# Kernel tuning notes

Measured on AMD Instinct MI355X. Metric: run time of the kernel, lower is better.

Reference implementation:

```python
import jax, jax.numpy as jnp
import numpy as np

N = 20000
E = 320000
IN_FEAT = 256
HID = 256
OUT_FEAT = 128


def setup_inputs() -> dict:
    key = jax.random.key(0)
    ks = jax.random.split(key, 10)
    inp = {
        "x": jax.random.normal(ks[0], (N, IN_FEAT), dtype=jnp.float32),
        "edge_src": jax.random.randint(ks[1], (E,), 0, N, dtype=jnp.int32),
        "edge_dst": jax.random.randint(ks[2], (E,), 0, N, dtype=jnp.int32),
        "edge_w": jax.random.uniform(ks[3], (E,), dtype=jnp.float32),
        # params (Linear weights stored as [out, in], torch convention)
        "W_emb": jax.random.normal(ks[4], (HID, IN_FEAT), dtype=jnp.float32) / np.sqrt(IN_FEAT),
        "W_gc1": jax.random.normal(ks[5], (HID, 2 * HID), dtype=jnp.float32) / np.sqrt(2 * HID),
        "b_gc1": jnp.zeros((HID,), dtype=jnp.float32),
        "W_gc2": jax.random.normal(ks[6], (HID, 2 * HID), dtype=jnp.float32) / np.sqrt(2 * HID),
        "b_gc2": jnp.zeros((HID,), dtype=jnp.float32),
        "W_fc": jax.random.normal(ks[7], (OUT_FEAT, HID), dtype=jnp.float32) / np.sqrt(HID),
    }
    return inp


def reference(x, edge_src, edge_dst, edge_w, W_emb, W_gc1, b_gc1, W_gc2, b_gc2, W_fc):
    n = x.shape[0]

    def adj_mul(h):
        msgs = h[edge_src] * edge_w[:, None]           # [E, hid]
        return jax.ops.segment_sum(msgs, edge_dst, num_segments=n)

    def gconv(h, W, b):
        cat = jnp.concatenate([h, adj_mul(h)], axis=1)  # [N, 2*hid]
        return cat @ W.T + b

    h = x @ W_emb.T                                    # embedding (no bias)
    h = h + jax.nn.relu(gconv(h, W_gc1, b_gc1))        # residual (dropout = eval identity)
    h = h + jax.nn.relu(gconv(h, W_gc2, b_gc2))
    out = h @ W_fc.T                                   # fc_last (no bias)
    out = out / jnp.sqrt(jnp.sum(out * out, axis=1, keepdims=True))
    return out
```

## Files before the change

### kernel.cpp

```cpp
#include <hip/hip_runtime.h>
#include <math.h>

#define N_NODES 20000
#define E_EDGES 320000
#define HID 256
#define OUT_FEAT 128
#define MPAD 20224
#define CAP 64

#define BK 64
#define LSTR 72
#define ISTR 80
#define TSTR 264

typedef __attribute__((ext_vector_type(8))) __bf16 bf16x8;
typedef __attribute__((ext_vector_type(4))) float floatx4;
typedef __attribute__((ext_vector_type(4))) int intx4;

__device__ __forceinline__ void write_int8_shadow(
    const __bf16 (*tile)[TSTR], int row0, int tid,
    unsigned char* __restrict__ h8, float* __restrict__ scl) {
    const int row = tid >> 3;
    const int seg = tid & 7;
    float vals[32];
    float mx = 0.f;
#pragma unroll
    for (int j = 0; j < 32; j++) {
        float v = (float)tile[row][seg * 32 + j];
        vals[j] = v;
        mx = fmaxf(mx, fabsf(v));
    }
#pragma unroll
    for (int m = 1; m <= 4; m <<= 1) mx = fmaxf(mx, __shfl_xor(mx, m));
    const float enc = mx > 0.f ? 127.f / mx : 0.f;
    unsigned int pk[8];
#pragma unroll
    for (int g = 0; g < 8; g++) {
        unsigned int wd = 0;
#pragma unroll
        for (int j = 0; j < 4; j++) {
            int q = (int)rintf(vals[g * 4 + j] * enc);
            q = q > 127 ? 127 : (q < -127 ? -127 : q);
            wd |= ((unsigned int)(q & 0xff)) << (8 * j);
        }
        pk[g] = wd;
    }
    unsigned char* dstp = h8 + (size_t)(row0 + row) * HID + seg * 32;
    *(int4*)dstp        = make_int4(pk[0], pk[1], pk[2], pk[3]);
    *(int4*)(dstp + 16) = make_int4(pk[4], pk[5], pk[6], pk[7]);
    if (seg == 0) scl[row0 + row] = mx * (1.f / 127.f);
}


#define EMB_BLK 316
#define SCAT_BLK 625
#define CONVL_BLK 40
#define CONVR_BLK 64

__global__ __launch_bounds__(512) void front_kernel(
    const float* __restrict__ x, const float* __restrict__ wembf,
    __bf16* __restrict__ hb0, unsigned char* __restrict__ h8, float* __restrict__ scl,
    const int* __restrict__ src, const int* __restrict__ dst,
    const float* __restrict__ w, int* __restrict__ counts, int2* __restrict__ edges,
    const float* __restrict__ w1f, const float* __restrict__ w2f, const float* __restrict__ wfcf,
    __bf16* __restrict__ w1l, __bf16* __restrict__ w2l, __bf16* __restrict__ wfcb,
    unsigned char* __restrict__ w1r8, unsigned char* __restrict__ w2r8,
    float* __restrict__ w1rs, float* __restrict__ w2rs)
{
    __shared__ char smem[64 * 144 + 256 * 144];
    const int bid = blockIdx.x;
    const int tid = threadIdx.x;

    if (bid < EMB_BLK) {
        __bf16* As = (__bf16*)smem;
        __bf16* Bs = (__bf16*)(smem + 64 * 144);
        const int row0 = bid * 64;
        const int wv = tid >> 6, l = tid & 63, lr = l & 15, lq = l >> 4;
        const int wm = wv & 1, wn4 = wv >> 1;

        floatx4 acc[2][4];
#pragma unroll
        for (int i = 0; i < 2; i++)
#pragma unroll
            for (int j = 0; j < 4; j++) acc[i][j] = (floatx4){0.f, 0.f, 0.f, 0.f};

        const int srow = tid >> 3;
        const int skq = (tid & 7) * 8;

        for (int kc = 0; kc < 256; kc += BK) {
            {
                int grow = row0 + srow;
                float4 v0 = make_float4(0.f, 0.f, 0.f, 0.f), v1 = v0;
                if (grow < N_NODES) {
                    const float* xp = x + (size_t)grow * HID + kc + skq;
                    v0 = *(const float4*)xp;
                    v1 = *(const float4*)(xp + 4);
                }
                bf16x8 o;
                o[0] = (__bf16)v0.x; o[1] = (__bf16)v0.y; o[2] = (__bf16)v0.z; o[3] = (__bf16)v0.w;
                o[4] = (__bf16)v1.x; o[5] = (__bf16)v1.y; o[6] = (__bf16)v1.z; o[7] = (__bf16)v1.w;
                *(bf16x8*)&As[srow * LSTR + skq] = o;
            }
#pragma unroll
            for (int r = 0; r < 4; r++) {
                int row = r * 64 + srow;
                const float* wp = wembf + (size_t)row * 256 + kc + skq;
                float4 v0 = *(const float4*)wp;
                float4 v1 = *(const float4*)(wp + 4);
                bf16x8 o;
                o[0] = (__bf16)v0.x; o[1] = (__bf16)v0.y; o[2] = (__bf16)v0.z; o[3] = (__bf16)v0.w;
                o[4] = (__bf16)v1.x; o[5] = (__bf16)v1.y; o[6] = (__bf16)v1.z; o[7] = (__bf16)v1.w;
                *(bf16x8*)&Bs[row * LSTR + skq] = o;
            }
            __syncthreads();
#pragma unroll
            for (int s = 0; s < 2; s++) {
                bf16x8 af[2], bfr[4];
#pragma unroll
                for (int mt = 0; mt < 2; mt++)
                    af[mt] = *(const bf16x8*)&As[(wm * 32 + mt * 16 + lr) * LSTR + s * 32 + lq * 8];
#pragma unroll
                for (int nt = 0; nt < 4; nt++)
                    bfr[nt] = *(const bf16x8*)&Bs[(wn4 * 64 + nt * 16 + lr) * LSTR + s * 32 + lq * 8];
#pragma unroll
                for (int mt = 0; mt < 2; mt++)
#pragma unroll
                    for (int nt = 0; nt < 4; nt++)
                        acc[mt][nt] = __builtin_amdgcn_mfma_f32_16x16x32_bf16(af[mt], bfr[nt], acc[mt][nt], 0, 0, 0);
            }
            __syncthreads();
        }
        __bf16 (*tile)[TSTR] = (__bf16(*)[TSTR])smem;
#pragma unroll
        for (int nt = 0; nt < 4; nt++) {
            const int col = wn4 * 64 + nt * 16 + lr;
#pragma unroll
            for (int mt = 0; mt < 2; mt++) {
                const int lrow = wm * 32 + mt * 16 + lq * 4;
#pragma unroll
                for (int r = 0; r < 4; r++) {
                    float v = acc[mt][nt][r];
                    hb0[(size_t)(row0 + lrow + r) * HID + col] = (__bf16)v;
                    tile[lrow + r][col] = (__bf16)v;
                }
            }
        }
        __syncthreads();
        write_int8_shadow(tile, row0, tid, h8, scl);
    } else if (bid < EMB_BLK + SCAT_BLK) {
        int e = (bid - EMB_BLK) * 512 + tid;
        int d = dst[e];
        int p = atomicAdd(&counts[d], 1);
        edges[(size_t)d * CAP + p] = make_int2(src[e], __float_as_int(w[e]));
    } else if (bid < EMB_BLK + SCAT_BLK + CONVL_BLK) {
        const size_t gi = ((size_t)(bid - EMB_BLK - SCAT_BLK) * 512 + tid) * 8;
        const float* sp; __bf16* dp;
        if (gi < 65536) {
            size_t row = gi >> 8, k = gi & 255;
            sp = w1f + row * 512 + k; dp = w1l + gi;
        } else if (gi < 131072) {
            size_t off = gi - 65536, row = off >> 8, k = off & 255;
            sp = w2f + row * 512 + k; dp = w2l + off;
        } else {
            size_t off = gi - 131072;
            sp = wfcf + off; dp = wfcb + off;
        }
        float4 v0 = *(const float4*)sp;
        float4 v1 = *(const float4*)(sp + 4);
        bf16x8 o;
        o[0] = (__bf16)v0.x; o[1] = (__bf16)v0.y; o[2] = (__bf16)v0.z; o[3] = (__bf16)v0.w;
        o[4] = (__bf16)v1.x; o[5] = (__bf16)v1.y; o[6] = (__bf16)v1.z; o[7] = (__bf16)v1.w;
        *(bf16x8*)dp = o;
    } else {
        const int gw = (bid - EMB_BLK - SCAT_BLK - CONVL_BLK) * 8 + (tid >> 6);
        const int lane = tid & 63;
        const float* Wsrc = (gw < 256) ? w1f : w2f;
        unsigned char* d8 = (gw < 256) ? w1r8 : w2r8;
        float* ds = (gw < 256) ? w1rs : w2rs;
        const int r = gw & 255;
        float4 v = *(const float4*)(Wsrc + (size_t)r * 512 + 256 + lane * 4);
        float mx = fmaxf(fmaxf(fabsf(v.x), fabsf(v.y)), fmaxf(fabsf(v.z), fabsf(v.w)));
#pragma unroll
        for (int m = 1; m <= 32; m <<= 1) mx = fmaxf(mx, __shfl_xor(mx, m));
        const float enc = mx > 0.f ? 127.f / mx : 0.f;
        unsigned int wd = 0;
        float vv[4] = {v.x, v.y, v.z, v.w};
#pragma unroll
        for (int j = 0; j < 4; j++) {
            int q = (int)rintf(vv[j] * enc);
            q = q > 127 ? 127 : (q < -127 ? -127 : q);
            wd |= ((unsigned int)(q & 0xff)) << (8 * j);
        }
        *(unsigned int*)(d8 + (size_t)r * 256 + lane * 4) = wd;
        if (lane == 0) ds[r] = mx * (1.f / 127.f);
    }
}


__global__ __launch_bounds__(256) void aggregate_kernel(
    const unsigned char* __restrict__ h8, const float* __restrict__ scl,
    const int* __restrict__ counts,
    const int2* __restrict__ edges,
    unsigned char* __restrict__ agg8, float* __restrict__ ascl) {
    const int w = threadIdx.x >> 6, lane = threadIdx.x & 63;
    const int half = lane >> 5, lh = lane & 31;
    const int d = blockIdx.x * 8 + w * 2 + half;
    const size_t base = (size_t)d * CAP;
    const int cnt = counts[d];
    const int iters = (cnt + 15) >> 4;
    float acc[8];
#pragma unroll
    for (int q = 0; q < 8; q++) acc[q] = 0.f;

    for (int it = 0; it < iters; ++it) {
        const int jb = it * 16;
        const int2* ep = edges + base + jb;
        int4 eh[8];
#pragma unroll
        for (int u = 0; u < 8; u++) eh[u] = *(const int4*)(ep + u * 2);
        int sidx[16]; float ew[16];
#pragma unroll
        for (int u = 0; u < 8; u++) {
            const bool m0 = (jb + u * 2)     < cnt;
            const bool m1 = (jb + u * 2 + 1) < cnt;
            sidx[u * 2]     = m0 ? eh[u].x : 0;
            ew[u * 2]       = m0 ? __int_as_float(eh[u].y) : 0.f;
            sidx[u * 2 + 1] = m1 ? eh[u].z : 0;
            ew[u * 2 + 1]   = m1 ? __int_as_float(eh[u].w) : 0.f;
        }
        float ws[16];
#pragma unroll
        for (int u = 0; u < 16; u++) ws[u] = ew[u] * scl[sidx[u]];
        uint2 hv[16];
#pragma unroll
        for (int u = 0; u < 16; u++)
            hv[u] = *(const uint2*)(h8 + (size_t)sidx[u] * HID + lh * 8);
#pragma unroll
        for (int u = 0; u < 16; u++) {
            const unsigned int a = hv[u].x, b = hv[u].y;
            const float wu = ws[u];
            acc[0] = fmaf(wu, (float)(int)(signed char)(a),       acc[0]);
            acc[1] = fmaf(wu, (float)(int)(signed char)(a >> 8),  acc[1]);
            acc[2] = fmaf(wu, (float)(int)(signed char)(a >> 16), acc[2]);
            acc[3] = fmaf(wu, (float)(int)(signed char)(a >> 24), acc[3]);
            acc[4] = fmaf(wu, (float)(int)(signed char)(b),       acc[4]);
            acc[5] = fmaf(wu, (float)(int)(signed char)(b >> 8),  acc[5]);
            acc[6] = fmaf(wu, (float)(int)(signed char)(b >> 16), acc[6]);
            acc[7] = fmaf(wu, (float)(int)(signed char)(b >> 24), acc[7]);
        }
    }
    float mx = 0.f;
#pragma unroll
    for (int q = 0; q < 8; q++) mx = fmaxf(mx, fabsf(acc[q]));
#pragma unroll
    for (int m = 1; m <= 16; m <<= 1) mx = fmaxf(mx, __shfl_xor(mx, m));
    const float enc = mx > 0.f ? 127.f / mx : 0.f;
    unsigned int w0 = 0, w1v = 0;
#pragma unroll
    for (int j = 0; j < 4; j++) {
        int q0 = (int)rintf(acc[j] * enc);
        q0 = q0 > 127 ? 127 : (q0 < -127 ? -127 : q0);
        w0 |= ((unsigned int)(q0 & 0xff)) << (8 * j);
        int q1 = (int)rintf(acc[4 + j] * enc);
        q1 = q1 > 127 ? 127 : (q1 < -127 ? -127 : q1);
        w1v |= ((unsigned int)(q1 & 0xff)) << (8 * j);
    }
    *(uint2*)(agg8 + (size_t)d * HID + lh * 8) = make_uint2(w0, w1v);
    if (lh == 0) ascl[d] = mx * (1.f / 127.f);
}


template <bool LAST>
__global__ __launch_bounds__(512) void gconv_kernel(
    const __bf16* __restrict__ hp,
    const unsigned char* __restrict__ ag8, const float* __restrict__ ascl,
    const __bf16* __restrict__ Wl,
    const unsigned char* __restrict__ Wr8, const float* __restrict__ Wrs,
    const float* __restrict__ bias,
    __bf16* __restrict__ hn, unsigned char* __restrict__ h8, float* __restrict__ scl,
    const __bf16* __restrict__ Wfc, float* __restrict__ outp)
{
    __shared__ char smem[64 * 144 + 256 * 144];
    __bf16* As = (__bf16*)smem;
    __bf16* Bs = (__bf16*)(smem + 64 * 144);
    char* As8 = smem;
    char* Bs8 = smem + 64 * ISTR;
    const int tid = threadIdx.x;
    const int row0 = blockIdx.x * 64;
    const int wv = tid >> 6, l = tid & 63, lr = l & 15, lq = l >> 4;
    const int wm = wv & 1, wn4 = wv >> 1;

    floatx4 acc[2][4];
    intx4 acc8[2][4];
#pragma unroll
    for (int i = 0; i < 2; i++)
#pragma unroll
        for (int j = 0; j < 4; j++) {
            acc[i][j] = (floatx4){0.f, 0.f, 0.f, 0.f};
            acc8[i][j] = (intx4){0, 0, 0, 0};
        }

    const int srow = tid >> 3;
    const int skq = (tid & 7) * 8;

    for (int kc = 0; kc < 256; kc += BK) {
        *(bf16x8*)&As[srow * LSTR + skq] =
            *(const bf16x8*)(hp + (size_t)(row0 + srow) * HID + kc + skq);
#pragma unroll
        for (int r = 0; r < 4; r++) {
            int row = r * 64 + srow;
            *(bf16x8*)&Bs[row * LSTR + skq] =
                *(const bf16x8*)(Wl + (size_t)row * 256 + kc + skq);
        }
        __syncthreads();
#pragma unroll
        for (int s = 0; s < 2; s++) {
            bf16x8 af[2], bfr[4];
#pragma unroll
            for (int mt = 0; mt < 2; mt++)
                af[mt] = *(const bf16x8*)&As[(wm * 32 + mt * 16 + lr) * LSTR + s * 32 + lq * 8];
#pragma unroll
            for (int nt = 0; nt < 4; nt++)
                bfr[nt] = *(const bf16x8*)&Bs[(wn4 * 64 + nt * 16 + lr) * LSTR + s * 32 + lq * 8];
#pragma unroll
            for (int mt = 0; mt < 2; mt++)
#pragma unroll
                for (int nt = 0; nt < 4; nt++)
                    acc[mt][nt] = __builtin_amdgcn_mfma_f32_16x16x32_bf16(af[mt], bfr[nt], acc[mt][nt], 0, 0, 0);
        }
        __syncthreads();
    }

    for (int kc = 0; kc < 256; kc += BK) {
        {
            int row = tid >> 3, sg = (tid & 7) * 8;
            *(uint2*)&As8[row * ISTR + sg] =
                *(const uint2*)(ag8 + (size_t)(row0 + row) * HID + kc + sg);
        }
#pragma unroll
        for (int rr = 0; rr < 2; rr++) {
            int idx = rr * 512 + tid;
            int row = idx >> 2, sg = (idx & 3) * 16;
            *(int4*)&Bs8[row * ISTR + sg] =
                *(const int4*)(Wr8 + (size_t)row * 256 + kc + sg);
        }
        __syncthreads();
        intx4 a8[2], b8[4];
#pragma unroll
        for (int mt = 0; mt < 2; mt++)
            a8[mt] = *(const intx4*)&As8[(wm * 32 + mt * 16 + lr) * ISTR + lq * 16];
#pragma unroll
        for (int nt = 0; nt < 4; nt++)
            b8[nt] = *(const intx4*)&Bs8[(wn4 * 64 + nt * 16 + lr) * ISTR + lq * 16];
#pragma unroll
        for (int mt = 0; mt < 2; mt++)
#pragma unroll
            for (int nt = 0; nt < 4; nt++)
                acc8[mt][nt] = __builtin_amdgcn_mfma_i32_16x16x64_i8(a8[mt], b8[nt], acc8[mt][nt], 0, 0, 0);
        __syncthreads();
    }

    __bf16 (*tile)[TSTR] = (__bf16(*)[TSTR])smem;
#pragma unroll
    for (int nt = 0; nt < 4; nt++) {
        const int col = wn4 * 64 + nt * 16 + lr;
        const float b = bias[col];
        const float wrc = Wrs[col];
#pragma unroll
        for (int mt = 0; mt < 2; mt++) {
            const int lrow = wm * 32 + mt * 16 + lq * 4;
#pragma unroll
            for (int r = 0; r < 4; r++) {
                const int row = row0 + lrow + r;
                float gem = acc[mt][nt][r] + (float)acc8[mt][nt][r] * (ascl[row] * wrc);
                float res = (float)hp[(size_t)row * HID + col];
                float v = res + fmaxf(gem + b, 0.f);
                if (!LAST) hn[(size_t)row * HID + col] = (__bf16)v;
                tile[lrow + r][col] = (__bf16)v;
            }
        }
    }
    __syncthreads();

    if (!LAST) {
        write_int8_shadow(tile, row0, tid, h8, scl);
    } else if (wv < 4) {
        floatx4 facc[8];
#pragma unroll
        for (int j = 0; j < 8; j++) facc[j] = (floatx4){0.f, 0.f, 0.f, 0.f};
#pragma unroll
        for (int kt = 0; kt < 256; kt += 32) {
            bf16x8 a = *(const bf16x8*)&tile[wv * 16 + lr][kt + lq * 8];
            bf16x8 bf8[8];
#pragma unroll
            for (int nt = 0; nt < 8; nt++)
                bf8[nt] = *(const bf16x8*)(Wfc + (size_t)(nt * 16 + lr) * 256 + kt + lq * 8);
#pragma unroll
            for (int nt = 0; nt < 8; nt++)
                facc[nt] = __builtin_amdgcn_mfma_f32_16x16x32_bf16(a, bf8[nt], facc[nt], 0, 0, 0);
        }
        float s[4];
#pragma unroll
        for (int r = 0; r < 4; r++) {
            float t = 0.f;
#pragma unroll
            for (int nt = 0; nt < 8; nt++) t = fmaf(facc[nt][r], facc[nt][r], t);
            s[r] = t;
        }
#pragma unroll
        for (int mask = 1; mask <= 8; mask <<= 1) {
#pragma unroll
            for (int r = 0; r < 4; r++) s[r] += __shfl_xor(s[r], mask);
        }
        float inv[4];
#pragma unroll
        for (int r = 0; r < 4; r++) inv[r] = rsqrtf(s[r]);
#pragma unroll
        for (int r = 0; r < 4; r++) {
            int row = row0 + wv * 16 + lq * 4 + r;
            if (row >= N_NODES) continue;
#pragma unroll
            for (int nt = 0; nt < 8; nt++)
                outp[(size_t)row * OUT_FEAT + nt * 16 + lr] = facc[nt][r] * inv[r];
        }
    }
}


extern "C" void kernel_launch(void* const* d_in, const int* in_sizes, int n_in,
                              void* d_out, int out_size, void* d_ws, size_t ws_size,
                              hipStream_t stream) {
    const float* x        = (const float*)d_in[0];
    const int*   edge_src = (const int*)d_in[1];
    const int*   edge_dst = (const int*)d_in[2];
    const float* edge_w   = (const float*)d_in[3];
    const float* W_emb    = (const float*)d_in[4];
    const float* W_gc1    = (const float*)d_in[5];
    const float* b_gc1    = (const float*)d_in[6];
    const float* W_gc2    = (const float*)d_in[7];
    const float* b_gc2    = (const float*)d_in[8];
    const float* W_fc     = (const float*)d_in[9];
    float* out = (float*)d_out;

    char* p = (char*)d_ws;
    const size_t HROW = (size_t)MPAD * HID;
    __bf16* hb0   = (__bf16*)p;             p += HROW * 2;
    __bf16* hb1   = (__bf16*)p;             p += HROW * 2;
    unsigned char* h8 = (unsigned char*)p;  p += HROW;
    float*  scl   = (float*)p;              p += (size_t)MPAD * 4;
    unsigned char* agg8 = (unsigned char*)p; p += HROW;
    float*  ascl  = (float*)p;              p += (size_t)MPAD * 4;
    __bf16* w1l   = (__bf16*)p;             p += 65536 * 2;
    __bf16* w2l   = (__bf16*)p;             p += 65536 * 2;
    __bf16* wfcb  = (__bf16*)p;             p += 32768 * 2;
    unsigned char* w1r8 = (unsigned char*)p; p += 65536;
    unsigned char* w2r8 = (unsigned char*)p; p += 65536;
    float*  w1rs  = (float*)p;              p += 256 * 4;
    float*  w2rs  = (float*)p;              p += 256 * 4;
    int2*   edges = (int2*)p;               p += (size_t)N_NODES * CAP * 8;
    int*    counts = (int*)p;               p += (size_t)MPAD * 4;

    hipMemsetAsync(counts, 0, (size_t)MPAD * 4, stream);

    front_kernel<<<EMB_BLK + SCAT_BLK + CONVL_BLK + CONVR_BLK, 512, 0, stream>>>(
        x, W_emb, hb0, h8, scl, edge_src, edge_dst, edge_w, counts, edges,
        W_gc1, W_gc2, W_fc, w1l, w2l, wfcb, w1r8, w2r8, w1rs, w2rs);

    aggregate_kernel<<<N_NODES / 8, 256, 0, stream>>>(h8, scl, counts, edges, agg8, ascl);

    gconv_kernel<false><<<MPAD / 64, 512, 0, stream>>>(
        hb0, agg8, ascl, w1l, w1r8, w1rs, b_gc1, hb1, h8, scl, nullptr, nullptr);

    aggregate_kernel<<<N_NODES / 8, 256, 0, stream>>>(h8, scl, counts, edges, agg8, ascl);

    gconv_kernel<true><<<MPAD / 64, 512, 0, stream>>>(
        hb1, agg8, ascl, w2l, w2r8, w2rs, b_gc2, nullptr, nullptr, nullptr, wfcb, out);
}
```

Baseline: 203.1 us.

## Fuse edge aggregation into gconv kernel and drop LDS staging for GEMM

Removes the separate aggregate kernels. Each gconv block now gathers and aggregates its own 32 destination rows, quantizes the result to int8 and writes it straight into shared memory as the A operand of the int8 MFMA, so the agg8/ascl global round trip and two launches go away. The dense GEMM operands (hp, Wl, Wr8) are now loaded directly from global memory into registers instead of being staged through LDS. The block shrinks to 32 rows and 256 threads with an occupancy hint, and ping-pong int8 shadow buffers avoid a read/write race across blocks. The cost is less weight reuse per block and more global/L2 traffic for the weights, and the irregular gather now runs in the same kernel as the MFMA work.

Result: slower. 207.6 us (+2.2%).

```diff
diff --git a/kernel.cpp b/kernel.cpp
--- a/kernel.cpp
+++ b/kernel.cpp
@@ -197,98 +197,101 @@
 }
 
 
-__global__ __launch_bounds__(256) void aggregate_kernel(
-    const unsigned char* __restrict__ h8, const float* __restrict__ scl,
-    const int* __restrict__ counts,
-    const int2* __restrict__ edges,
-    unsigned char* __restrict__ agg8, float* __restrict__ ascl) {
-    const int w = threadIdx.x >> 6, lane = threadIdx.x & 63;
-    const int half = lane >> 5, lh = lane & 31;
-    const int d = blockIdx.x * 8 + w * 2 + half;
-    const size_t base = (size_t)d * CAP;
-    const int cnt = counts[d];
-    const int iters = (cnt + 15) >> 4;
-    float acc[8];
-#pragma unroll
-    for (int q = 0; q < 8; q++) acc[q] = 0.f;
-
-    for (int it = 0; it < iters; ++it) {
-        const int jb = it * 16;
-        const int2* ep = edges + base + jb;
-        int4 eh[8];
-#pragma unroll
-        for (int u = 0; u < 8; u++) eh[u] = *(const int4*)(ep + u * 2);
-        int sidx[16]; float ew[16];
-#pragma unroll
-        for (int u = 0; u < 8; u++) {
-            const bool m0 = (jb + u * 2)     < cnt;
-            const bool m1 = (jb + u * 2 + 1) < cnt;
-            sidx[u * 2]     = m0 ? eh[u].x : 0;
-            ew[u * 2]       = m0 ? __int_as_float(eh[u].y) : 0.f;
-            sidx[u * 2 + 1] = m1 ? eh[u].z : 0;
-            ew[u * 2 + 1]   = m1 ? __int_as_float(eh[u].w) : 0.f;
-        }
-        float ws[16];
-#pragma unroll
-        for (int u = 0; u < 16; u++) ws[u] = ew[u] * scl[sidx[u]];
-        uint2 hv[16];
-#pragma unroll
-        for (int u = 0; u < 16; u++)
-            hv[u] = *(const uint2*)(h8 + (size_t)sidx[u] * HID + lh * 8);
-#pragma unroll
-        for (int u = 0; u < 16; u++) {
-            const unsigned int a = hv[u].x, b = hv[u].y;
-            const float wu = ws[u];
-            acc[0] = fmaf(wu, (float)(int)(signed char)(a),       acc[0]);
-            acc[1] = fmaf(wu, (float)(int)(signed char)(a >> 8),  acc[1]);
-            acc[2] = fmaf(wu, (float)(int)(signed char)(a >> 16), acc[2]);
-            acc[3] = fmaf(wu, (float)(int)(signed char)(a >> 24), acc[3]);
-            acc[4] = fmaf(wu, (float)(int)(signed char)(b),       acc[4]);
-            acc[5] = fmaf(wu, (float)(int)(signed char)(b >> 8),  acc[5]);
-            acc[6] = fmaf(wu, (float)(int)(signed char)(b >> 16), acc[6]);
-            acc[7] = fmaf(wu, (float)(int)(signed char)(b >> 24), acc[7]);
-        }
-    }
-    float mx = 0.f;
-#pragma unroll
-    for (int q = 0; q < 8; q++) mx = fmaxf(mx, fabsf(acc[q]));
-#pragma unroll
-    for (int m = 1; m <= 16; m <<= 1) mx = fmaxf(mx, __shfl_xor(mx, m));
-    const float enc = mx > 0.f ? 127.f / mx : 0.f;
-    unsigned int w0 = 0, w1v = 0;
-#pragma unroll
-    for (int j = 0; j < 4; j++) {
-        int q0 = (int)rintf(acc[j] * enc);
-        q0 = q0 > 127 ? 127 : (q0 < -127 ? -127 : q0);
-        w0 |= ((unsigned int)(q0 & 0xff)) << (8 * j);
-        int q1 = (int)rintf(acc[4 + j] * enc);
-        q1 = q1 > 127 ? 127 : (q1 < -127 ? -127 : q1);
-        w1v |= ((unsigned int)(q1 & 0xff)) << (8 * j);
-    }
-    *(uint2*)(agg8 + (size_t)d * HID + lh * 8) = make_uint2(w0, w1v);
-    if (lh == 0) ascl[d] = mx * (1.f / 127.f);
-}
-
+#define GBM 32
+#define AGG_BYTES (4 * GBM * ISTR)
+#define ASCL_OFF  AGG_BYTES
+#define GEMM_OFF  (AGG_BYTES + 128)
+#define TILE_BYTES (GBM * TSTR * 2)
 
 template <bool LAST>
-__global__ __launch_bounds__(512) void gconv_kernel(
+__global__ __launch_bounds__(256, 3) void gconv_kernel(
     const __bf16* __restrict__ hp,
-    const unsigned char* __restrict__ ag8, const float* __restrict__ ascl,
+    const unsigned char* __restrict__ h8in, const float* __restrict__ sclin,
+    const int* __restrict__ counts, const int2* __restrict__ edges,
     const __bf16* __restrict__ Wl,
     const unsigned char* __restrict__ Wr8, const float* __restrict__ Wrs,
     const float* __restrict__ bias,
-    __bf16* __restrict__ hn, unsigned char* __restrict__ h8, float* __restrict__ scl,
+    __bf16* __restrict__ hn, unsigned char* __restrict__ h8out, float* __restrict__ sclout,
     const __bf16* __restrict__ Wfc, float* __restrict__ outp)
 {
-    __shared__ char smem[64 * 144 + 256 * 144];
-    __bf16* As = (__bf16*)smem;
-    __bf16* Bs = (__bf16*)(smem + 64 * 144);
+    __shared__ char smem[GEMM_OFF + TILE_BYTES];
     char* As8 = smem;
-    char* Bs8 = smem + 64 * ISTR;
+    float* asclL = (float*)(smem + ASCL_OFF);
     const int tid = threadIdx.x;
-    const int row0 = blockIdx.x * 64;
+    const int row0 = blockIdx.x * GBM;
     const int wv = tid >> 6, l = tid & 63, lr = l & 15, lq = l >> 4;
-    const int wm = wv & 1, wn4 = wv >> 1;
+
+    {
+        const int hw = tid >> 5;
+        const int lh = tid & 31;
+#pragma unroll 1
+        for (int t = 0; t < 4; ++t) {
+            const int j = hw * 4 + t;
+            const int d = row0 + j;
+            const size_t base = (size_t)d * CAP;
+            const int cnt = counts[d];
+            const int iters = (cnt + 15) >> 4;
+            float acc[8];
+#pragma unroll
+            for (int q = 0; q < 8; q++) acc[q] = 0.f;
+
+            for (int it = 0; it < iters; ++it) {
+                const int jb = it * 16;
+                const int2* ep = edges + base + jb;
+                int4 eh[8];
+#pragma unroll
+                for (int u = 0; u < 8; u++) eh[u] = *(const int4*)(ep + u * 2);
+                int sidx[16]; float ew[16];
+#pragma unroll
+                for (int u = 0; u < 8; u++) {
+                    const bool m0 = (jb + u * 2)     < cnt;
+                    const bool m1 = (jb + u * 2 + 1) < cnt;
+                    sidx[u * 2]     = m0 ? eh[u].x : 0;
+                    ew[u * 2]       = m0 ? __int_as_float(eh[u].y) : 0.f;
+                    sidx[u * 2 + 1] = m1 ? eh[u].z : 0;
+                    ew[u * 2 + 1]   = m1 ? __int_as_float(eh[u].w) : 0.f;
+                }
+                float ws[16];
+#pragma unroll
+                for (int u = 0; u < 16; u++) ws[u] = ew[u] * sclin[sidx[u]];
+                uint2 hv[16];
+#pragma unroll
+                for (int u = 0; u < 16; u++)
+                    hv[u] = *(const uint2*)(h8in + (size_t)sidx[u] * HID + lh * 8);
+#pragma unroll
+                for (int u = 0; u < 16; u++) {
+                    const unsigned int a = hv[u].x, b = hv[u].y;
+                    const float wu = ws[u];
+                    acc[0] = fmaf(wu, (float)(int)(signed char)(a),       acc[0]);
+                    acc[1] = fmaf(wu, (float)(int)(signed char)(a >> 8),  acc[1]);
+                    acc[2] = fmaf(wu, (float)(int)(signed char)(a >> 16), acc[2]);
+                    acc[3] = fmaf(wu, (float)(int)(signed char)(a >> 24), acc[3]);
+                    acc[4] = fmaf(wu, (float)(int)(signed char)(b),       acc[4]);
+                    acc[5] = fmaf(wu, (float)(int)(signed char)(b >> 8),  acc[5]);
+                    acc[6] = fmaf(wu, (float)(int)(signed char)(b >> 16), acc[6]);
+                    acc[7] = fmaf(wu, (float)(int)(signed char)(b >> 24), acc[7]);
+                }
+            }
+            float mx = 0.f;
+#pragma unroll
+            for (int q = 0; q < 8; q++) mx = fmaxf(mx, fabsf(acc[q]));
+#pragma unroll
+            for (int m = 1; m <= 16; m <<= 1) mx = fmaxf(mx, __shfl_xor(mx, m));
+            const float enc = mx > 0.f ? 127.f / mx : 0.f;
+            unsigned int w0 = 0, w1v = 0;
+#pragma unroll
+            for (int jj = 0; jj < 4; jj++) {
+                int q0 = (int)rintf(acc[jj] * enc);
+                q0 = q0 > 127 ? 127 : (q0 < -127 ? -127 : q0);
+                w0 |= ((unsigned int)(q0 & 0xff)) << (8 * jj);
+                int q1 = (int)rintf(acc[4 + jj] * enc);
+                q1 = q1 > 127 ? 127 : (q1 < -127 ? -127 : q1);
+                w1v |= ((unsigned int)(q1 & 0xff)) << (8 * jj);
+            }
+            *(uint2*)&As8[(((lh >> 3) * GBM) + j) * ISTR + (lh & 7) * 8] = make_uint2(w0, w1v);
+            if (lh == 0) asclL[j] = mx * (1.f / 127.f);
+        }
+    }
 
     floatx4 acc[2][4];
     intx4 acc8[2][4];
@@ -300,79 +303,57 @@
             acc8[i][j] = (intx4){0, 0, 0, 0};
         }
 
-    const int srow = tid >> 3;
-    const int skq = (tid & 7) * 8;
-
+#pragma unroll
     for (int kc = 0; kc < 256; kc += BK) {
-        *(bf16x8*)&As[srow * LSTR + skq] =
-            *(const bf16x8*)(hp + (size_t)(row0 + srow) * HID + kc + skq);
-#pragma unroll
-        for (int r = 0; r < 4; r++) {
-            int row = r * 64 + srow;
-            *(bf16x8*)&Bs[row * LSTR + skq] =
-                *(const bf16x8*)(Wl + (size_t)row * 256 + kc + skq);
-        }
-        __syncthreads();
 #pragma unroll
         for (int s = 0; s < 2; s++) {
+            const int k0 = kc + s * 32 + lq * 8;
             bf16x8 af[2], bfr[4];
 #pragma unroll
             for (int mt = 0; mt < 2; mt++)
-                af[mt] = *(const bf16x8*)&As[(wm * 32 + mt * 16 + lr) * LSTR + s * 32 + lq * 8];
+                af[mt] = *(const bf16x8*)(hp + (size_t)(row0 + mt * 16 + lr) * HID + k0);
 #pragma unroll
             for (int nt = 0; nt < 4; nt++)
-                bfr[nt] = *(const bf16x8*)&Bs[(wn4 * 64 + nt * 16 + lr) * LSTR + s * 32 + lq * 8];
+                bfr[nt] = *(const bf16x8*)(Wl + (size_t)(wv * 64 + nt * 16 + lr) * 256 + k0);
 #pragma unroll
             for (int mt = 0; mt < 2; mt++)
 #pragma unroll
                 for (int nt = 0; nt < 4; nt++)
                     acc[mt][nt] = __builtin_amdgcn_mfma_f32_16x16x32_bf16(af[mt], bfr[nt], acc[mt][nt], 0, 0, 0);
         }
-        __syncthreads();
-    }
-
+    }
+
+    __syncthreads();
+
+#pragma unroll
     for (int kc = 0; kc < 256; kc += BK) {
-        {
-            int row = tid >> 3, sg = (tid & 7) * 8;
-            *(uint2*)&As8[row * ISTR + sg] =
-                *(const uint2*)(ag8 + (size_t)(row0 + row) * HID + kc + sg);
-        }
-#pragma unroll
-        for (int rr = 0; rr < 2; rr++) {
-            int idx = rr * 512 + tid;
-            int row = idx >> 2, sg = (idx & 3) * 16;
-            *(int4*)&Bs8[row * ISTR + sg] =
-                *(const int4*)(Wr8 + (size_t)row * 256 + kc + sg);
-        }
-        __syncthreads();
         intx4 a8[2], b8[4];
 #pragma unroll
         for (int mt = 0; mt < 2; mt++)
-            a8[mt] = *(const intx4*)&As8[(wm * 32 + mt * 16 + lr) * ISTR + lq * 16];
+            a8[mt] = *(const intx4*)&As8[(((kc >> 6) * GBM) + mt * 16 + lr) * ISTR + lq * 16];
 #pragma unroll
         for (int nt = 0; nt < 4; nt++)
-            b8[nt] = *(const intx4*)&Bs8[(wn4 * 64 + nt * 16 + lr) * ISTR + lq * 16];
+            b8[nt] = *(const intx4*)(Wr8 + (size_t)(wv * 64 + nt * 16 + lr) * 256 + kc + lq * 16);
 #pragma unroll
         for (int mt = 0; mt < 2; mt++)
 #pragma unroll
             for (int nt = 0; nt < 4; nt++)
                 acc8[mt][nt] = __builtin_amdgcn_mfma_i32_16x16x64_i8(a8[mt], b8[nt], acc8[mt][nt], 0, 0, 0);
-        __syncthreads();
-    }
-
-    __bf16 (*tile)[TSTR] = (__bf16(*)[TSTR])smem;
+    }
+
+    __bf16 (*tile)[TSTR] = (__bf16(*)[TSTR])(smem + GEMM_OFF);
 #pragma unroll
     for (int nt = 0; nt < 4; nt++) {
-        const int col = wn4 * 64 + nt * 16 + lr;
+        const int col = wv * 64 + nt * 16 + lr;
         const float b = bias[col];
         const float wrc = Wrs[col];
 #pragma unroll
         for (int mt = 0; mt < 2; mt++) {
-            const int lrow = wm * 32 + mt * 16 + lq * 4;
+            const int lrow = mt * 16 + lq * 4;
 #pragma unroll
             for (int r = 0; r < 4; r++) {
                 const int row = row0 + lrow + r;
-                float gem = acc[mt][nt][r] + (float)acc8[mt][nt][r] * (ascl[row] * wrc);
+                float gem = acc[mt][nt][r] + (float)acc8[mt][nt][r] * (asclL[lrow + r] * wrc);
                 float res = (float)hp[(size_t)row * HID + col];
                 float v = res + fmaxf(gem + b, 0.f);
                 if (!LAST) hn[(size_t)row * HID + col] = (__bf16)v;
@@ -383,8 +364,8 @@
     __syncthreads();
 
     if (!LAST) {
-        write_int8_shadow(tile, row0, tid, h8, scl);
-    } else if (wv < 4) {
+        write_int8_shadow(tile, row0, tid, h8out, sclout);
+    } else if (wv < 2) {
         floatx4 facc[8];
 #pragma unroll
         for (int j = 0; j < 8; j++) facc[j] = (floatx4){0.f, 0.f, 0.f, 0.f};
@@ -446,10 +427,10 @@
     const size_t HROW = (size_t)MPAD * HID;
     __bf16* hb0   = (__bf16*)p;             p += HROW * 2;
     __bf16* hb1   = (__bf16*)p;             p += HROW * 2;
-    unsigned char* h8 = (unsigned char*)p;  p += HROW;
-    float*  scl   = (float*)p;              p += (size_t)MPAD * 4;
-    unsigned char* agg8 = (unsigned char*)p; p += HROW;
-    float*  ascl  = (float*)p;              p += (size_t)MPAD * 4;
+    unsigned char* h8a = (unsigned char*)p; p += HROW;
+    float*  scla  = (float*)p;              p += (size_t)MPAD * 4;
+    unsigned char* h8b = (unsigned char*)p; p += HROW;
+    float*  sclb  = (float*)p;              p += (size_t)MPAD * 4;
     __bf16* w1l   = (__bf16*)p;             p += 65536 * 2;
     __bf16* w2l   = (__bf16*)p;             p += 65536 * 2;
     __bf16* wfcb  = (__bf16*)p;             p += 32768 * 2;
@@ -463,16 +444,14 @@
     hipMemsetAsync(counts, 0, (size_t)MPAD * 4, stream);
 
     front_kernel<<<EMB_BLK + SCAT_BLK + CONVL_BLK + CONVR_BLK, 512, 0, stream>>>(
-        x, W_emb, hb0, h8, scl, edge_src, edge_dst, edge_w, counts, edges,
+        x, W_emb, hb0, h8a, scla, edge_src, edge_dst, edge_w, counts, edges,
         W_gc1, W_gc2, W_fc, w1l, w2l, wfcb, w1r8, w2r8, w1rs, w2rs);
 
-    aggregate_kernel<<<N_NODES / 8, 256, 0, stream>>>(h8, scl, counts, edges, agg8, ascl);
-
-    gconv_kernel<false><<<MPAD / 64, 512, 0, stream>>>(
-        hb0, agg8, ascl, w1l, w1r8, w1rs, b_gc1, hb1, h8, scl, nullptr, nullptr);
-
-    aggregate_kernel<<<N_NODES / 8, 256, 0, stream>>>(h8, scl, counts, edges, agg8, ascl);
-
-    gconv_kernel<true><<<MPAD / 64, 512, 0, stream>>>(
-        hb1, agg8, ascl, w2l, w2r8, w2rs, b_gc2, nullptr, nullptr, nullptr, wfcb, out);
+    gconv_kernel<false><<<MPAD / GBM, 256, 0, stream>>>(
+        hb0, h8a, scla, counts, edges, w1l, w1r8, w1rs, b_gc1,
+        hb1, h8b, sclb, nullptr, nullptr);
+
+    gconv_kernel<true><<<MPAD / GBM, 256, 0, stream>>>(
+        hb1, h8b, sclb, counts, edges, w2l, w2r8, w2rs, b_gc2,
+        nullptr, nullptr, nullptr, wfcb, out);
 }
```
